# Optimization experiments

Hardware: AMD Instinct MI355X
Metric: run time of the kernel (lower is better)

The kernel has to match this reference:

```python
import jax, jax.numpy as jnp
import numpy as np

INIT_W = 10.0
INIT_B = -5.0
N, M, D = 2048, 10, 256


def setup_inputs() -> dict:
    key = jax.random.key(0)
    k1, = jax.random.split(key, 1)
    embeddings = jax.random.normal(k1, (N, M, D), dtype=jnp.float32)
    w = jnp.asarray(INIT_W, dtype=jnp.float32)
    b = jnp.asarray(INIT_B, dtype=jnp.float32)
    return {"embeddings": embeddings, "w": w, "b": b}


def _l2norm(x, axis=-1, eps=1e-12):
    # matches torch F.normalize: x / max(||x||, eps)
    n = jnp.sqrt(jnp.sum(x * x, axis=axis, keepdims=True))
    return x / jnp.maximum(n, eps)


def reference(embeddings, w, b):
    # embeddings: (N, M, D)
    centroids = _l2norm(embeddings.mean(axis=1))          # (N, D)
    emb_norm = _l2norm(embeddings)                        # (N, M, D)
    sim = jnp.einsum('nmd,kd->nmk', emb_norm, centroids)  # (N, M, N)
    sim = sim * jnp.abs(w) + b
    # cross-entropy with target n for every (n, m):
    # loss = mean_{n,m} [ logsumexp_k sim[n,m,k] - sim[n,m,n] ]
    lse = jax.nn.logsumexp(sim, axis=-1)                  # (N, M)
    pos = jnp.take_along_axis(
        sim, jnp.arange(sim.shape[0])[:, None, None], axis=-1
    )[..., 0]                                             # (N, M)
    return jnp.mean(lse - pos)
```

## Files before the change

kernel.cpp:

```cpp
#include <hip/hip_runtime.h>
#include <hip/hip_bf16.h>

#define N_SPK 2048
#define M_UTT 10
#define D_DIM 256
#define NM (N_SPK * M_UTT)

typedef __attribute__((ext_vector_type(8))) short bf16x8_t;
typedef __attribute__((ext_vector_type(16))) float f32x16_t;

__device__ __forceinline__ short f2bf(float x) {
  __hip_bfloat16 h = __float2bfloat16(x);
  return *reinterpret_cast<short*>(&h);
}

__global__ __launch_bounds__(256) void k_prep(const float* __restrict__ emb,
                                              __hip_bfloat16* __restrict__ Bf,
                                              __hip_bfloat16* __restrict__ embn,
                                              float* __restrict__ dvals,
                                              float* __restrict__ rowsum,
                                              float* __restrict__ out) {
  const int n = blockIdx.x, d = threadIdx.x;
  const int wid = d >> 6, lane = d & 63;
  const float* p = emb + (size_t)n * (M_UTT * D_DIM) + d;

  float e[M_UTT];
  float s = 0.f;
#pragma unroll
  for (int m = 0; m < M_UTT; ++m) { e[m] = p[m * D_DIM]; s += e[m]; }

  float ss = s * s;
#pragma unroll
  for (int o = 32; o >= 1; o >>= 1) ss += __shfl_xor(ss, o, 64);
  __shared__ float redc[4];
  if (lane == 0) redc[wid] = ss;
  __syncthreads();
  float tot = redc[0] + redc[1] + redc[2] + redc[3];
  float inv = 1.0f / fmaxf(sqrtf(tot), 1e-11f);
  float v = s * inv;

  int idx = (((n >> 5) * 16 + (d >> 4)) * 64 + ((d >> 3) & 1) * 32 + (n & 31)) * 8 + (d & 7);
  Bf[idx] = __float2bfloat16(v);

  __shared__ float redm[M_UTT][2][4];
#pragma unroll
  for (int m = 0; m < M_UTT; ++m) {
    float a = e[m] * e[m], bb = e[m] * v;
#pragma unroll
    for (int o = 32; o >= 1; o >>= 1) {
      a += __shfl_xor(a, o, 64);
      bb += __shfl_xor(bb, o, 64);
    }
    if (lane == 0) { redm[m][0][wid] = a; redm[m][1][wid] = bb; }
  }
  __syncthreads();
  __shared__ float rnb[M_UTT];
  if (d < M_UTT) {
    float ssm = redm[d][0][0] + redm[d][0][1] + redm[d][0][2] + redm[d][0][3];
    float dtm = redm[d][1][0] + redm[d][1][1] + redm[d][1][2] + redm[d][1][3];
    float rn = 1.0f / fmaxf(sqrtf(ssm), 1e-12f);
    rnb[d] = rn;
    dvals[n * M_UTT + d] = dtm * rn;
    rowsum[n * M_UTT + d] = 0.f;
  }
  if (n == 0 && d == 0) out[0] = 0.f;
  __syncthreads();

  short* eo = (short*)embn + (size_t)n * (M_UTT * D_DIM) + d;
#pragma unroll
  for (int m = 0; m < M_UTT; ++m) eo[m * D_DIM] = f2bf(e[m] * rnb[m]);
}

__global__ __launch_bounds__(512, 2) void k_gemm(const __hip_bfloat16* __restrict__ embn,
                                                 const __hip_bfloat16* __restrict__ Bf,
                                                 float* __restrict__ rowsum,
                                                 const float* __restrict__ wp) {
  __shared__ short As[128 * 256];
  const float aw = fabsf(wp[0]);
  const int tid = threadIdx.x;
  const int lane = tid & 63, w = tid >> 6;
  const int l31 = lane & 31, lh = lane >> 5;
  const int row0 = blockIdx.x * 128;

  {
    const short* srcbase = (const short*)embn;
#pragma unroll
    for (int p = 0; p < 8; ++p) {
      int r = p * 16 + w * 2 + lh;
      const short* src = srcbase + (size_t)(row0 + r) * D_DIM + ((l31 ^ (r & 7)) << 3);
      __builtin_amdgcn_global_load_lds(
          (const __attribute__((address_space(1))) void*)src,
          (__attribute__((address_space(3))) void*)&As[p * 4096 + w * 512],
          16, 0, 0);
    }
  }
  asm volatile("s_waitcnt vmcnt(0)" ::: "memory");
  __syncthreads();

  const int cg = blockIdx.y * 16 + w * 2;
  const bf16x8_t* b0p = (const bf16x8_t*)Bf + (size_t)(cg * 16) * 64 + lane;
  const bf16x8_t* b1p = (const bf16x8_t*)Bf + (size_t)((cg + 1) * 16) * 64 + lane;

  f32x16_t acc[4][2];
#pragma unroll
  for (int rg = 0; rg < 4; ++rg)
#pragma unroll
    for (int ci = 0; ci < 2; ++ci)
#pragma unroll
      for (int r = 0; r < 16; ++r) acc[rg][ci][r] = 0.f;

  bf16x8_t cb0 = b0p[0], cb1 = b1p[0];
  bf16x8_t e0, e1, e2, e3;
  {
    const int sw = (lh ^ (l31 & 7)) << 3;
    e0 = *(const bf16x8_t*)&As[l31 * 256 + sw];
    e1 = *(const bf16x8_t*)&As[(l31 + 32) * 256 + sw];
    e2 = *(const bf16x8_t*)&As[(l31 + 64) * 256 + sw];
    e3 = *(const bf16x8_t*)&As[(l31 + 96) * 256 + sw];
  }

#pragma unroll
  for (int ks = 0; ks < 16; ++ks) {
    bf16x8_t nb0, nb1, f0, f1, f2, f3;
    if (ks < 15) {
      nb0 = b0p[(ks + 1) * 64];
      nb1 = b1p[(ks + 1) * 64];
      const int sw = (((ks + 1) * 2 + lh) ^ (l31 & 7)) << 3;
      f0 = *(const bf16x8_t*)&As[l31 * 256 + sw];
      f1 = *(const bf16x8_t*)&As[(l31 + 32) * 256 + sw];
      f2 = *(const bf16x8_t*)&As[(l31 + 64) * 256 + sw];
      f3 = *(const bf16x8_t*)&As[(l31 + 96) * 256 + sw];
    }
    acc[0][0] = __builtin_amdgcn_mfma_f32_32x32x16_bf16(cb0, e0, acc[0][0], 0, 0, 0);
    acc[0][1] = __builtin_amdgcn_mfma_f32_32x32x16_bf16(cb1, e0, acc[0][1], 0, 0, 0);
    acc[1][0] = __builtin_amdgcn_mfma_f32_32x32x16_bf16(cb0, e1, acc[1][0], 0, 0, 0);
    acc[1][1] = __builtin_amdgcn_mfma_f32_32x32x16_bf16(cb1, e1, acc[1][1], 0, 0, 0);
    acc[2][0] = __builtin_amdgcn_mfma_f32_32x32x16_bf16(cb0, e2, acc[2][0], 0, 0, 0);
    acc[2][1] = __builtin_amdgcn_mfma_f32_32x32x16_bf16(cb1, e2, acc[2][1], 0, 0, 0);
    acc[3][0] = __builtin_amdgcn_mfma_f32_32x32x16_bf16(cb0, e3, acc[3][0], 0, 0, 0);
    acc[3][1] = __builtin_amdgcn_mfma_f32_32x32x16_bf16(cb1, e3, acc[3][1], 0, 0, 0);
    cb0 = nb0; cb1 = nb1;
    e0 = f0; e1 = f1; e2 = f2; e3 = f3;
  }

#pragma unroll
  for (int rg = 0; rg < 4; ++rg) {
    float s = 0.f;
#pragma unroll
    for (int ci = 0; ci < 2; ++ci)
#pragma unroll
      for (int r = 0; r < 16; ++r)
        s += __expf(fmaf(aw, acc[rg][ci][r], -aw));
    s += __shfl_xor(s, 32, 64);
    if (lane < 32) atomicAdd(&rowsum[row0 + rg * 32 + lane], s);
  }
}

__global__ __launch_bounds__(256) void k_final(const float* __restrict__ rowsum,
                                               const float* __restrict__ dvals,
                                               const float* __restrict__ wp,
                                               float* __restrict__ out) {
  const float aw = fabsf(wp[0]);
  int base = blockIdx.x * 512 + threadIdx.x;
  float c = 0.f;
#pragma unroll
  for (int j = 0; j < 2; ++j) {
    int r = base + j * 256;
    c += logf(rowsum[r]) + aw * (1.0f - dvals[r]);
  }
#pragma unroll
  for (int o = 32; o >= 1; o >>= 1) c += __shfl_xor(c, o, 64);
  __shared__ float rs[4];
  int wid = threadIdx.x >> 6, lane = threadIdx.x & 63;
  if (lane == 0) rs[wid] = c;
  __syncthreads();
  if (threadIdx.x == 0)
    atomicAdd(out, (rs[0] + rs[1] + rs[2] + rs[3]) * (1.0f / (float)NM));
}

extern "C" void kernel_launch(void* const* d_in, const int* in_sizes, int n_in,
                              void* d_out, int out_size, void* d_ws, size_t ws_size,
                              hipStream_t stream) {
  const float* emb = (const float*)d_in[0];
  const float* wp  = (const float*)d_in[1];
  float* out = (float*)d_out;

  char* ws = (char*)d_ws;
  float* rowsum = (float*)(ws);
  float* dvals  = (float*)(ws + (128 << 10));
  __hip_bfloat16* Bf   = (__hip_bfloat16*)(ws + (1 << 20));
  __hip_bfloat16* embn = (__hip_bfloat16*)(ws + (2 << 20));

  k_prep<<<N_SPK, 256, 0, stream>>>(emb, Bf, embn, dvals, rowsum, out);
  k_gemm<<<dim3(NM / 128, 4), 512, 0, stream>>>(embn, Bf, rowsum, wp);
  k_final<<<NM / 512, 256, 0, stream>>>(rowsum, dvals, wp, out);
}
```

Baseline: 110.0 us.

## Drop LDS staging in GEMM; load A rows into registers with 2x2 warp tiling

Result: slower. 129.6 us (+17.8%).

```diff
diff --git a/kernel.cpp b/kernel.cpp
--- a/kernel.cpp
+++ b/kernel.cpp
@@ -75,76 +75,53 @@
                                                  const __hip_bfloat16* __restrict__ Bf,
                                                  float* __restrict__ rowsum,
                                                  const float* __restrict__ wp) {
-  __shared__ short As[128 * 256];
   const float aw = fabsf(wp[0]);
   const int tid = threadIdx.x;
   const int lane = tid & 63, w = tid >> 6;
   const int l31 = lane & 31, lh = lane >> 5;
-  const int row0 = blockIdx.x * 128;
+  const int wr = w >> 1, wc = w & 1;
+  const int row0 = blockIdx.x * 256 + wr * 64;
+  const int cg0 = blockIdx.y * 4 + wc * 2;
 
-  {
-    const short* srcbase = (const short*)embn;
+  const bf16x8_t* bp0 = (const bf16x8_t*)Bf + (size_t)(cg0 * 16) * 64 + lane;
+  const bf16x8_t* bp1 = (const bf16x8_t*)Bf + (size_t)((cg0 + 1) * 16) * 64 + lane;
+
+  bf16x8_t cb0[3], cb1[3];
 #pragma unroll
-    for (int p = 0; p < 8; ++p) {
-      int r = p * 16 + w * 2 + lh;
-      const short* src = srcbase + (size_t)(row0 + r) * D_DIM + ((l31 ^ (r & 7)) << 3);
-      __builtin_amdgcn_global_load_lds(
-          (const __attribute__((address_space(1))) void*)src,
-          (__attribute__((address_space(3))) void*)&As[p * 4096 + w * 512],
-          16, 0, 0);
-    }
+  for (int p = 0; p < 3; ++p) { cb0[p] = bp0[p * 64]; cb1[p] = bp1[p * 64]; }
+
+  bf16x8_t breg[2][16];
+#pragma unroll
+  for (int rg = 0; rg < 2; ++rg) {
+    const bf16x8_t* rowp =
+        (const bf16x8_t*)embn + (size_t)(row0 + rg * 32 + l31) * 32 + lh;
+#pragma unroll
+    for (int ks = 0; ks < 16; ++ks) breg[rg][ks] = rowp[ks * 2];
   }
-  asm volatile("s_waitcnt vmcnt(0)" ::: "memory");
-  __syncthreads();
 
-  const int cg = blockIdx.y * 16 + w * 2;
-  const bf16x8_t* b0p = (const bf16x8_t*)Bf + (size_t)(cg * 16) * 64 + lane;
-  const bf16x8_t* b1p = (const bf16x8_t*)Bf + (size_t)((cg + 1) * 16) * 64 + lane;
-
-  f32x16_t acc[4][2];
+  f32x16_t acc[2][2];
 #pragma unroll
-  for (int rg = 0; rg < 4; ++rg)
+  for (int rg = 0; rg < 2; ++rg)
 #pragma unroll
     for (int ci = 0; ci < 2; ++ci)
 #pragma unroll
       for (int r = 0; r < 16; ++r) acc[rg][ci][r] = 0.f;
 
-  bf16x8_t cb0 = b0p[0], cb1 = b1p[0];
-  bf16x8_t e0, e1, e2, e3;
-  {
-    const int sw = (lh ^ (l31 & 7)) << 3;
-    e0 = *(const bf16x8_t*)&As[l31 * 256 + sw];
-    e1 = *(const bf16x8_t*)&As[(l31 + 32) * 256 + sw];
-    e2 = *(const bf16x8_t*)&As[(l31 + 64) * 256 + sw];
-    e3 = *(const bf16x8_t*)&As[(l31 + 96) * 256 + sw];
+#pragma unroll
+  for (int ks = 0; ks < 16; ++ks) {
+    bf16x8_t b0 = cb0[ks % 3], b1 = cb1[ks % 3];
+    if (ks + 3 < 16) {
+      cb0[ks % 3] = bp0[(ks + 3) * 64];
+      cb1[ks % 3] = bp1[(ks + 3) * 64];
+    }
+    acc[0][0] = __builtin_amdgcn_mfma_f32_32x32x16_bf16(b0, breg[0][ks], acc[0][0], 0, 0, 0);
+    acc[0][1] = __builtin_amdgcn_mfma_f32_32x32x16_bf16(b1, breg[0][ks], acc[0][1], 0, 0, 0);
+    acc[1][0] = __builtin_amdgcn_mfma_f32_32x32x16_bf16(b0, breg[1][ks], acc[1][0], 0, 0, 0);
+    acc[1][1] = __builtin_amdgcn_mfma_f32_32x32x16_bf16(b1, breg[1][ks], acc[1][1], 0, 0, 0);
   }
 
 #pragma unroll
-  for (int ks = 0; ks < 16; ++ks) {
-    bf16x8_t nb0, nb1, f0, f1, f2, f3;
-    if (ks < 15) {
-      nb0 = b0p[(ks + 1) * 64];
-      nb1 = b1p[(ks + 1) * 64];
-      const int sw = (((ks + 1) * 2 + lh) ^ (l31 & 7)) << 3;
-      f0 = *(const bf16x8_t*)&As[l31 * 256 + sw];
-      f1 = *(const bf16x8_t*)&As[(l31 + 32) * 256 + sw];
-      f2 = *(const bf16x8_t*)&As[(l31 + 64) * 256 + sw];
-      f3 = *(const bf16x8_t*)&As[(l31 + 96) * 256 + sw];
-    }
-    acc[0][0] = __builtin_amdgcn_mfma_f32_32x32x16_bf16(cb0, e0, acc[0][0], 0, 0, 0);
-    acc[0][1] = __builtin_amdgcn_mfma_f32_32x32x16_bf16(cb1, e0, acc[0][1], 0, 0, 0);
-    acc[1][0] = __builtin_amdgcn_mfma_f32_32x32x16_bf16(cb0, e1, acc[1][0], 0, 0, 0);
-    acc[1][1] = __builtin_amdgcn_mfma_f32_32x32x16_bf16(cb1, e1, acc[1][1], 0, 0, 0);
-    acc[2][0] = __builtin_amdgcn_mfma_f32_32x32x16_bf16(cb0, e2, acc[2][0], 0, 0, 0);
-    acc[2][1] = __builtin_amdgcn_mfma_f32_32x32x16_bf16(cb1, e2, acc[2][1], 0, 0, 0);
-    acc[3][0] = __builtin_amdgcn_mfma_f32_32x32x16_bf16(cb0, e3, acc[3][0], 0, 0, 0);
-    acc[3][1] = __builtin_amdgcn_mfma_f32_32x32x16_bf16(cb1, e3, acc[3][1], 0, 0, 0);
-    cb0 = nb0; cb1 = nb1;
-    e0 = f0; e1 = f1; e2 = f2; e3 = f3;
-  }
-
-#pragma unroll
-  for (int rg = 0; rg < 4; ++rg) {
+  for (int rg = 0; rg < 2; ++rg) {
     float s = 0.f;
 #pragma unroll
     for (int ci = 0; ci < 2; ++ci)
@@ -192,6 +169,6 @@
   __hip_bfloat16* embn = (__hip_bfloat16*)(ws + (2 << 20));
 
   k_prep<<<N_SPK, 256, 0, stream>>>(emb, Bf, embn, dvals, rowsum, out);
-  k_gemm<<<dim3(NM / 128, 4), 512, 0, stream>>>(embn, Bf, rowsum, wp);
+  k_gemm<<<dim3(NM / 256, 16), 512, 0, stream>>>(embn, Bf, rowsum, wp);
   k_final<<<NM / 512, 256, 0, stream>>>(rowsum, dvals, wp, out);
 }
```
